# Kernel tuning notes

Measured on AMD Instinct MI355X. Metric: run time of the kernel, lower is better.

Reference implementation:

```python
import jax, jax.numpy as jnp
import numpy as np

D_MODEL = 1024
EXPANDED = 1024  # d_model * expansion_factor(1.0)
K = 3
EPS = 1e-8


def rms_norm(x, w, eps=EPS):
    return x * jax.lax.rsqrt(jnp.mean(x * x, axis=-1, keepdims=True) + eps) * w


def setup_inputs() -> dict:
    key = jax.random.key(0)
    ks = jax.random.split(key, 8)
    b, t = 4, 4096
    u = jax.random.normal(ks[0], (b, t, D_MODEL), dtype=jnp.float32)
    s_in = 1.0 / np.sqrt(D_MODEL)
    s_out = 1.0 / np.sqrt(EXPANDED)
    W_in = jax.random.uniform(ks[1], (2 * EXPANDED, D_MODEL), jnp.float32, -s_in, s_in)
    b_in = jax.random.uniform(ks[2], (2 * EXPANDED,), jnp.float32, -s_in, s_in)
    in_norm_w = jnp.ones((2 * EXPANDED,), jnp.float32)
    s_conv = 1.0 / np.sqrt(K)  # groups=expanded_dim -> fan_in = K
    conv_w = jax.random.uniform(ks[3], (EXPANDED, 1, K), jnp.float32, -s_conv, s_conv)
    conv_b = jax.random.uniform(ks[4], (EXPANDED,), jnp.float32, -s_conv, s_conv)
    W_out = jax.random.uniform(ks[5], (D_MODEL, EXPANDED), jnp.float32, -s_out, s_out)
    b_out = jax.random.uniform(ks[6], (D_MODEL,), jnp.float32, -s_out, s_out)
    out_norm_w = jnp.ones((D_MODEL,), jnp.float32)
    return {
        "u": u, "W_in": W_in, "b_in": b_in, "in_norm_w": in_norm_w,
        "conv_w": conv_w, "conv_b": conv_b,
        "W_out": W_out, "b_out": b_out, "out_norm_w": out_norm_w,
    }


def reference(u, W_in, b_in, in_norm_w, conv_w, conv_b, W_out, b_out, out_norm_w):
    # in_proj + RMSNorm
    xv = rms_norm(jnp.einsum('btd,ed->bte', u, W_in) + b_in, in_norm_w)  # [b,t,2E]
    x, v = jnp.split(xv, 2, axis=-1)  # each [b,t,E]
    # depthwise 'same' conv along time: NCH layout
    x_f = jnp.transpose(x, (0, 2, 1))  # [b,E,t]
    pad = (K - 1) // 2
    y = jax.lax.conv_general_dilated(
        x_f, conv_w, window_strides=(1,), padding=[(pad, pad)],
        dimension_numbers=('NCH', 'OIH', 'NCH'), feature_group_count=EXPANDED)
    y = y + conv_b[None, :, None]
    x_mixed = jnp.transpose(y, (0, 2, 1))  # [b,t,E]
    gated = v * x_mixed
    out = rms_norm(jnp.einsum('bte,de->btd', gated, W_out) + b_out, out_norm_w)
    return out
```

## Files before the change

kernel.cpp:

```cpp
#include <hip/hip_runtime.h>

#define BT    16384
#define TSEQ  4096
#define DM    1024
#define EXP   1024
#define N1    2048
#define KDIM  1024
#define NKT   (KDIM / 64)
#define EPSV  1e-8f

typedef __bf16 bf16x8 __attribute__((ext_vector_type(8)));
typedef float f32x16 __attribute__((ext_vector_type(16)));
typedef unsigned short u16x8 __attribute__((ext_vector_type(8)));

#define AS1CAST(p) ((__attribute__((address_space(1))) void*)(p))
#define AS3CAST(p) ((__attribute__((address_space(3))) void*)(p))

__device__ __forceinline__ unsigned short f2bf(float f) {
    unsigned int u = __float_as_uint(f);
    u += 0x7fffu + ((u >> 16) & 1u);
    return (unsigned short)(u >> 16);
}

__global__ __launch_bounds__(256) void k_f2bf3(const float* __restrict__ i0, unsigned short* __restrict__ o0, int n0,
                                               const float* __restrict__ i1, unsigned short* __restrict__ o1, int n1,
                                               const float* __restrict__ i2, unsigned short* __restrict__ o2, int n2) {
    int i = blockIdx.x * 256 + threadIdx.x;
    const float* in; unsigned short* out;
    if (i < n0)                { in = i0; out = o0; }
    else if (i < n0 + n1)      { in = i1; out = o1; i -= n0; }
    else if (i < n0 + n1 + n2) { in = i2; out = o2; i -= n0 + n1; }
    else return;
    float4 v = ((const float4*)in)[i];
    ushort4 o;
    o.x = f2bf(v.x); o.y = f2bf(v.y); o.z = f2bf(v.z); o.w = f2bf(v.w);
    ((ushort4*)out)[i] = o;
}

template <int BF16_OUT>
__device__ __forceinline__ void gemm_body(const unsigned short* __restrict__ A,
                                          const unsigned short* __restrict__ Bw,
                                          const float* __restrict__ bias,
                                          unsigned short* __restrict__ Cb,
                                          float* __restrict__ Cf,
                                          float* __restrict__ ssq,
                                          int N) {
    __shared__ unsigned short sB[128 * 64];

    const int tid  = threadIdx.x;
    const int lane = tid & 63;
    const int w    = tid >> 6;
    const int ln   = lane & 31;
    const int hi   = lane >> 5;
    const int row0 = blockIdx.y * 256, col0 = blockIdx.x * 128;

    const unsigned short* aRow0 = A + (size_t)(row0 + w * 64 + ln) * KDIM + hi * 8;
    const unsigned short* aRow1 = aRow0 + (size_t)32 * KDIM;

    const int r_b = tid >> 3;
    const int q_b = ((tid & 7) - r_b) & 7;
    const unsigned short* bSrc = Bw + (size_t)(col0 + r_b) * KDIM + q_b * 8;

    f32x16 acc[2][4] = {};

    auto loadA = [&](bf16x8* ar, int kt) {
#pragma unroll
        for (int ks = 0; ks < 4; ++ks) {
            ar[ks]     = *(const bf16x8*)(aRow0 + kt * 64 + ks * 16);
            ar[4 + ks] = *(const bf16x8*)(aRow1 + kt * 64 + ks * 16);
        }
    };
    auto stageB = [&](int kt) {
#pragma unroll
        for (int b = 0; b < 4; ++b)
            __builtin_amdgcn_global_load_lds(AS1CAST(bSrc + (size_t)b * 32 * KDIM + kt * 64),
                                             AS3CAST(&sB[(b * 256 + w * 64) * 8]), 16, 0, 0);
    };
    auto compute = [&](const bf16x8* ar) {
#pragma unroll
        for (int ks = 0; ks < 4; ++ks) {
            const int sw = ((ks * 2 + hi + ln) & 7) * 8;
            bf16x8 bF[4];
#pragma unroll
            for (int j = 0; j < 4; ++j)
                bF[j] = *(const bf16x8*)&sB[(j * 32 + ln) * 64 + sw];
#pragma unroll
            for (int i = 0; i < 2; ++i)
#pragma unroll
                for (int j = 0; j < 4; ++j)
                    acc[i][j] = __builtin_amdgcn_mfma_f32_32x32x16_bf16(
                        ar[i * 4 + ks], bF[j], acc[i][j], 0, 0, 0);
        }
    };

    bf16x8 a0[8], a1[8];
    loadA(a0, 0);
    for (int kt = 0; kt < NKT; kt += 2) {
        __syncthreads();
        stageB(kt);
        __syncthreads();
        loadA(a1, kt + 1);
        compute(a0);
        __syncthreads();
        stageB(kt + 1);
        __syncthreads();
        loadA(a0, (kt + 2 < NKT) ? kt + 2 : 0);
        compute(a1);
    }

    const int c0 = col0 + ln;
    float bs[4];
#pragma unroll
    for (int j = 0; j < 4; ++j) bs[j] = bias[c0 + j * 32];

#pragma unroll
    for (int i = 0; i < 2; ++i) {
        const int rb = row0 + w * 64 + i * 32 + 4 * hi;
#pragma unroll
        for (int reg = 0; reg < 16; ++reg) {
            const int gm = rb + (reg & 3) + 8 * (reg >> 2);
            float v[4]; float p = 0.f;
#pragma unroll
            for (int j = 0; j < 4; ++j) {
                v[j] = acc[i][j][reg] + bs[j];
                p += v[j] * v[j];
            }
#pragma unroll
            for (int off = 1; off < 32; off <<= 1) p += __shfl_xor(p, off, 64);
            if (ln == 0) atomicAdd(&ssq[gm], p);
            size_t base = (size_t)gm * N + c0;
#pragma unroll
            for (int j = 0; j < 4; ++j) {
                if (BF16_OUT) Cb[base + j * 32] = f2bf(v[j]);
                else          Cf[base + j * 32] = v[j];
            }
        }
    }
}

__global__ __launch_bounds__(256, 2) void k_gemm_in(const unsigned short* __restrict__ A,
                                                    const unsigned short* __restrict__ Bw,
                                                    const float* __restrict__ bias,
                                                    unsigned short* __restrict__ Cb,
                                                    float* __restrict__ ssq) {
    gemm_body<1>(A, Bw, bias, Cb, nullptr, ssq, N1);
}

__global__ __launch_bounds__(256, 2) void k_gemm_out(const unsigned short* __restrict__ A,
                                                     const unsigned short* __restrict__ Bw,
                                                     const float* __restrict__ bias,
                                                     float* __restrict__ Cf,
                                                     float* __restrict__ ssq) {
    gemm_body<0>(A, Bw, bias, nullptr, Cf, ssq, DM);
}

__global__ __launch_bounds__(256) void k_conv_gate(const unsigned short* __restrict__ z,
                                                   const float* __restrict__ ssq1,
                                                   const float* __restrict__ inw,
                                                   const float* __restrict__ cw,
                                                   const float* __restrict__ cb,
                                                   unsigned short* __restrict__ g) {
    const int tok = blockIdx.x * 2 + (threadIdx.x >> 7);
    const int e8  = (threadIdx.x & 127) * 8;
    const int t   = tok & (TSEQ - 1);

    const float rs0 = rsqrtf(ssq1[tok] * (1.0f / N1) + EPSV);
    const int tm = (t > 0) ? tok - 1 : tok;
    const int tp = (t < TSEQ - 1) ? tok + 1 : tok;
    const float rsm = (t > 0) ? rsqrtf(ssq1[tm] * (1.0f / N1) + EPSV) : 0.0f;
    const float rsp = (t < TSEQ - 1) ? rsqrtf(ssq1[tp] * (1.0f / N1) + EPSV) : 0.0f;

    bf16x8 xm = *(const bf16x8*)(z + (size_t)tm * N1 + e8);
    bf16x8 x0 = *(const bf16x8*)(z + (size_t)tok * N1 + e8);
    bf16x8 xp = *(const bf16x8*)(z + (size_t)tp * N1 + e8);
    bf16x8 vv = *(const bf16x8*)(z + (size_t)tok * N1 + EXP + e8);

    u16x8 ov;
#pragma unroll
    for (int p = 0; p < 8; ++p) {
        const int e = e8 + p;
        const float we  = inw[e];
        const float wvv = inw[EXP + e];
        const float w0 = cw[e * 3], w1 = cw[e * 3 + 1], w2 = cw[e * 3 + 2];
        float y = w0 * ((float)xm[p] * rsm * we)
                + w1 * ((float)x0[p] * rs0 * we)
                + w2 * ((float)xp[p] * rsp * we)
                + cb[e];
        float vn = (float)vv[p] * rs0 * wvv;
        ov[p] = f2bf(vn * y);
    }
    *(u16x8*)(g + (size_t)tok * EXP + e8) = ov;
}

__global__ __launch_bounds__(256) void k_outnorm(float* __restrict__ o,
                                                 const float* __restrict__ ssq2,
                                                 const float* __restrict__ onw) {
    const int idx = blockIdx.x * 256 + threadIdx.x;
    const int tok = idx >> 8;
    const int d4  = (idx & 255) * 4;
    const float rs = rsqrtf(ssq2[tok] * (1.0f / DM) + EPSV);
    float4 v = ((float4*)o)[idx];
    float4 w = *(const float4*)(onw + d4);
    v.x *= rs * w.x; v.y *= rs * w.y; v.z *= rs * w.z; v.w *= rs * w.w;
    ((float4*)o)[idx] = v;
}

extern "C" void kernel_launch(void* const* d_in, const int* in_sizes, int n_in,
                              void* d_out, int out_size, void* d_ws, size_t ws_size,
                              hipStream_t stream) {
    const float* u     = (const float*)d_in[0];
    const float* W_in  = (const float*)d_in[1];
    const float* b_in  = (const float*)d_in[2];
    const float* inw   = (const float*)d_in[3];
    const float* cw    = (const float*)d_in[4];
    const float* cb    = (const float*)d_in[5];
    const float* W_out = (const float*)d_in[6];
    const float* b_out = (const float*)d_in[7];
    const float* onw   = (const float*)d_in[8];
    float* out = (float*)d_out;

    char* ws = (char*)d_ws;
    unsigned short* u_bf    = (unsigned short*)ws; ws += (size_t)BT * DM * 2;
    unsigned short* Win_bf  = (unsigned short*)ws; ws += (size_t)N1 * DM * 2;
    unsigned short* Wout_bf = (unsigned short*)ws; ws += (size_t)DM * EXP * 2;
    unsigned short* z_bf    = (unsigned short*)ws; ws += (size_t)BT * N1 * 2;
    unsigned short* g_bf    = (unsigned short*)ws; ws += (size_t)BT * EXP * 2;
    float* ssq1 = (float*)ws; ws += (size_t)BT * 4;
    float* ssq2 = (float*)ws; ws += (size_t)BT * 4;

    hipMemsetAsync(ssq1, 0, (size_t)BT * 2 * sizeof(float), stream);

    const int n0 = BT * DM / 4, n1c = N1 * DM / 4, n2c = DM * EXP / 4;
    k_f2bf3<<<(n0 + n1c + n2c + 255) / 256, 256, 0, stream>>>(u, u_bf, n0,
                                                              W_in, Win_bf, n1c,
                                                              W_out, Wout_bf, n2c);

    dim3 gA(N1 / 128, BT / 256);
    k_gemm_in<<<gA, 256, 0, stream>>>(u_bf, Win_bf, b_in, z_bf, ssq1);

    k_conv_gate<<<BT / 2, 256, 0, stream>>>(z_bf, ssq1, inw, cw, cb, g_bf);

    dim3 gC(DM / 128, BT / 256);
    k_gemm_out<<<gC, 256, 0, stream>>>(g_bf, Wout_bf, b_out, out, ssq2);

    k_outnorm<<<BT, 256, 0, stream>>>(out, ssq2, onw);

    (void)in_sizes; (void)n_in; (void)out_size; (void)ws_size;
}
```

Measured before the change: 354.4 us.

## Stage A tiles through LDS, swizzle block order, fold ssq zeroing into convert

Both GEMMs now load the A tile into shared memory with global_load_lds, as B already was, instead of each warp keeping A in registers through a two-stage register pipeline. Blocks use a 1D grid with a grouped mapping, 8 M-tiles per group sweeping all N-tiles, to improve L2 reuse of A and B. The separate memset of the norm accumulators is folded into the conversion kernel to save a launch. LDS use grows to 48KB per block and the register-level prefetch of A is lost, so load latency may be less hidden.

```diff
diff --git a/kernel.cpp b/kernel.cpp
--- a/kernel.cpp
+++ b/kernel.cpp
@@ -24,20 +24,25 @@
 
 __global__ __launch_bounds__(256) void k_f2bf3(const float* __restrict__ i0, unsigned short* __restrict__ o0, int n0,
                                                const float* __restrict__ i1, unsigned short* __restrict__ o1, int n1,
-                                               const float* __restrict__ i2, unsigned short* __restrict__ o2, int n2) {
+                                               const float* __restrict__ i2, unsigned short* __restrict__ o2, int n2,
+                                               float* __restrict__ ssq) {
     int i = blockIdx.x * 256 + threadIdx.x;
     const float* in; unsigned short* out;
     if (i < n0)                { in = i0; out = o0; }
     else if (i < n0 + n1)      { in = i1; out = o1; i -= n0; }
     else if (i < n0 + n1 + n2) { in = i2; out = o2; i -= n0 + n1; }
-    else return;
+    else {
+        i -= n0 + n1 + n2;
+        if (i < 2 * BT / 4) ((float4*)ssq)[i] = make_float4(0.f, 0.f, 0.f, 0.f);
+        return;
+    }
     float4 v = ((const float4*)in)[i];
     ushort4 o;
     o.x = f2bf(v.x); o.y = f2bf(v.y); o.z = f2bf(v.z); o.w = f2bf(v.w);
     ((ushort4*)out)[i] = o;
 }
 
-template <int BF16_OUT>
+template <int BF16_OUT, int NT>
 __device__ __forceinline__ void gemm_body(const unsigned short* __restrict__ A,
                                           const unsigned short* __restrict__ Bw,
                                           const float* __restrict__ bias,
@@ -45,6 +50,7 @@
                                           float* __restrict__ Cf,
                                           float* __restrict__ ssq,
                                           int N) {
+    __shared__ unsigned short sA[256 * 64];
     __shared__ unsigned short sB[128 * 64];
 
     const int tid  = threadIdx.x;
@@ -52,35 +58,38 @@
     const int w    = tid >> 6;
     const int ln   = lane & 31;
     const int hi   = lane >> 5;
-    const int row0 = blockIdx.y * 256, col0 = blockIdx.x * 128;
-
-    const unsigned short* aRow0 = A + (size_t)(row0 + w * 64 + ln) * KDIM + hi * 8;
-    const unsigned short* aRow1 = aRow0 + (size_t)32 * KDIM;
-
-    const int r_b = tid >> 3;
-    const int q_b = ((tid & 7) - r_b) & 7;
-    const unsigned short* bSrc = Bw + (size_t)(col0 + r_b) * KDIM + q_b * 8;
+
+    const int L   = blockIdx.x;
+    const int mt  = ((L >> 3) / NT) * 8 + (L & 7);
+    const int nt  = (L >> 3) & (NT - 1);
+    const int row0 = mt * 256, col0 = nt * 128;
+
+    const int rA = tid >> 3;
+    const int qS = ((tid & 7) - rA) & 7;
+    const unsigned short* aSrc = A  + (size_t)(row0 + rA) * KDIM + qS * 8;
+    const unsigned short* bSrc = Bw + (size_t)(col0 + rA) * KDIM + qS * 8;
 
     f32x16 acc[2][4] = {};
 
-    auto loadA = [&](bf16x8* ar, int kt) {
-#pragma unroll
-        for (int ks = 0; ks < 4; ++ks) {
-            ar[ks]     = *(const bf16x8*)(aRow0 + kt * 64 + ks * 16);
-            ar[4 + ks] = *(const bf16x8*)(aRow1 + kt * 64 + ks * 16);
-        }
-    };
-    auto stageB = [&](int kt) {
+    for (int kt = 0; kt < NKT; ++kt) {
+        __syncthreads();
+#pragma unroll
+        for (int b = 0; b < 8; ++b)
+            __builtin_amdgcn_global_load_lds(AS1CAST(aSrc + (size_t)b * 32 * KDIM + kt * 64),
+                                             AS3CAST(&sA[(b * 256 + w * 64) * 8]), 16, 0, 0);
 #pragma unroll
         for (int b = 0; b < 4; ++b)
             __builtin_amdgcn_global_load_lds(AS1CAST(bSrc + (size_t)b * 32 * KDIM + kt * 64),
                                              AS3CAST(&sB[(b * 256 + w * 64) * 8]), 16, 0, 0);
-    };
-    auto compute = [&](const bf16x8* ar) {
+        __syncthreads();
+
 #pragma unroll
         for (int ks = 0; ks < 4; ++ks) {
             const int sw = ((ks * 2 + hi + ln) & 7) * 8;
-            bf16x8 bF[4];
+            bf16x8 aF[2], bF[4];
+#pragma unroll
+            for (int i = 0; i < 2; ++i)
+                aF[i] = *(const bf16x8*)&sA[(w * 64 + i * 32 + ln) * 64 + sw];
 #pragma unroll
             for (int j = 0; j < 4; ++j)
                 bF[j] = *(const bf16x8*)&sB[(j * 32 + ln) * 64 + sw];
@@ -89,23 +98,8 @@
 #pragma unroll
                 for (int j = 0; j < 4; ++j)
                     acc[i][j] = __builtin_amdgcn_mfma_f32_32x32x16_bf16(
-                        ar[i * 4 + ks], bF[j], acc[i][j], 0, 0, 0);
+                        aF[i], bF[j], acc[i][j], 0, 0, 0);
         }
-    };
-
-    bf16x8 a0[8], a1[8];
-    loadA(a0, 0);
-    for (int kt = 0; kt < NKT; kt += 2) {
-        __syncthreads();
-        stageB(kt);
-        __syncthreads();
-        loadA(a1, kt + 1);
-        compute(a0);
-        __syncthreads();
-        stageB(kt + 1);
-        __syncthreads();
-        loadA(a0, (kt + 2 < NKT) ? kt + 2 : 0);
-        compute(a1);
     }
 
     const int c0 = col0 + ln;
@@ -143,7 +137,7 @@
                                                     const float* __restrict__ bias,
                                                     unsigned short* __restrict__ Cb,
                                                     float* __restrict__ ssq) {
-    gemm_body<1>(A, Bw, bias, Cb, nullptr, ssq, N1);
+    gemm_body<1, 16>(A, Bw, bias, Cb, nullptr, ssq, N1);
 }
 
 __global__ __launch_bounds__(256, 2) void k_gemm_out(const unsigned short* __restrict__ A,
@@ -151,7 +145,7 @@
                                                      const float* __restrict__ bias,
                                                      float* __restrict__ Cf,
                                                      float* __restrict__ ssq) {
-    gemm_body<0>(A, Bw, bias, nullptr, Cf, ssq, DM);
+    gemm_body<0, 8>(A, Bw, bias, nullptr, Cf, ssq, DM);
 }
 
 __global__ __launch_bounds__(256) void k_conv_gate(const unsigned short* __restrict__ z,
@@ -228,20 +222,18 @@
     float* ssq1 = (float*)ws; ws += (size_t)BT * 4;
     float* ssq2 = (float*)ws; ws += (size_t)BT * 4;
 
-    hipMemsetAsync(ssq1, 0, (size_t)BT * 2 * sizeof(float), stream);
-
     const int n0 = BT * DM / 4, n1c = N1 * DM / 4, n2c = DM * EXP / 4;
-    k_f2bf3<<<(n0 + n1c + n2c + 255) / 256, 256, 0, stream>>>(u, u_bf, n0,
-                                                              W_in, Win_bf, n1c,
-                                                              W_out, Wout_bf, n2c);
-
-    dim3 gA(N1 / 128, BT / 256);
-    k_gemm_in<<<gA, 256, 0, stream>>>(u_bf, Win_bf, b_in, z_bf, ssq1);
+    const int ntot = n0 + n1c + n2c + 2 * BT / 4;
+    k_f2bf3<<<(ntot + 255) / 256, 256, 0, stream>>>(u, u_bf, n0,
+                                                    W_in, Win_bf, n1c,
+                                                    W_out, Wout_bf, n2c,
+                                                    ssq1);
+
+    k_gemm_in<<<(BT / 256) * (N1 / 128), 256, 0, stream>>>(u_bf, Win_bf, b_in, z_bf, ssq1);
 
     k_conv_gate<<<BT / 2, 256, 0, stream>>>(z_bf, ssq1, inw, cw, cb, g_bf);
 
-    dim3 gC(DM / 128, BT / 256);
-    k_gemm_out<<<gC, 256, 0, stream>>>(g_bf, Wout_bf, b_out, out, ssq2);
+    k_gemm_out<<<(BT / 256) * (DM / 128), 256, 0, stream>>>(g_bf, Wout_bf, b_out, out, ssq2);
 
     k_outnorm<<<BT, 256, 0, stream>>>(out, ssq2, onw);
 
```

Measured after the change: 309.0 us. 12.8% less time.
